# Kernel tuning notes

Hardware: AMD Instinct MI355X
Metric: run time of the kernel (lower is better)

The kernel has to match this reference:

```python
import jax, jax.numpy as jnp
import numpy as np

N_ATOMS = 50000
N_EDGES = 1_600_000
N_MOL = 500
HIDDEN = 128
FILTERS = 128
GAUSS = 50
LAYERS = 3
CUTOFF = 10.0
LOG2 = 0.6931471805599453


def ssp(x):
    # ShiftedSoftplus: softplus(x) - log(2)
    return jax.nn.softplus(x) - LOG2


def setup_inputs() -> dict:
    key = jax.random.key(0)
    ks = jax.random.split(key, 24)
    z = jax.random.randint(ks[0], (N_ATOMS,), 0, 100)
    pos = jax.random.uniform(ks[1], (N_ATOMS, 3), jnp.float32) * 5.0  # box keeps d < cutoff
    batch = jnp.sort(jax.random.randint(ks[2], (N_ATOMS,), 0, N_MOL))
    row = jax.random.randint(ks[3], (N_EDGES,), 0, N_ATOMS)
    off = jax.random.randint(ks[4], (N_EDGES,), 1, N_ATOMS)
    col = (row + off) % N_ATOMS  # guarantees row != col (no zero distances)
    edge_index = jnp.stack([row, col])
    def lin(k, fi, fo):
        return jax.random.normal(k, (fi, fo), jnp.float32) * (1.0 / np.sqrt(fi))
    emb = jax.random.normal(ks[5], (100, HIDDEN), jnp.float32)
    mlp1_w = jnp.stack([lin(jax.random.fold_in(ks[6], i), GAUSS, FILTERS) for i in range(LAYERS)])
    mlp1_b = jnp.zeros((LAYERS, FILTERS), jnp.float32)
    mlp2_w = jnp.stack([lin(jax.random.fold_in(ks[7], i), FILTERS, FILTERS) for i in range(LAYERS)])
    mlp2_b = jnp.zeros((LAYERS, FILTERS), jnp.float32)
    lin1_w = jnp.stack([lin(jax.random.fold_in(ks[8], i), HIDDEN, FILTERS) for i in range(LAYERS)])
    lin2_w = jnp.stack([lin(jax.random.fold_in(ks[9], i), FILTERS, HIDDEN) for i in range(LAYERS)])
    lin2_b = jnp.zeros((LAYERS, HIDDEN), jnp.float32)
    int_w = jnp.stack([lin(jax.random.fold_in(ks[10], i), HIDDEN, HIDDEN) for i in range(LAYERS)])
    int_b = jnp.zeros((LAYERS, HIDDEN), jnp.float32)
    out1_w = lin(ks[11], HIDDEN, HIDDEN // 2)
    out1_b = jnp.zeros((HIDDEN // 2,), jnp.float32)
    out2_w = lin(ks[12], HIDDEN // 2, 1)
    out2_b = jnp.zeros((1,), jnp.float32)
    return {"z": z, "pos": pos, "batch": batch, "edge_index": edge_index,
            "emb": emb, "mlp1_w": mlp1_w, "mlp1_b": mlp1_b, "mlp2_w": mlp2_w, "mlp2_b": mlp2_b,
            "lin1_w": lin1_w, "lin2_w": lin2_w, "lin2_b": lin2_b, "int_w": int_w, "int_b": int_b,
            "out1_w": out1_w, "out1_b": out1_b, "out2_w": out2_w, "out2_b": out2_b}


def reference(z, pos, batch, edge_index, emb, mlp1_w, mlp1_b, mlp2_w, mlp2_b,
              lin1_w, lin2_w, lin2_b, int_w, int_b, out1_w, out1_b, out2_w, out2_b):
    row, col = edge_index[0], edge_index[1]  # source j, target i
    d = jnp.linalg.norm(pos[row] - pos[col], axis=-1)  # [E]
    # GaussianSmearing
    offset = jnp.linspace(0.0, CUTOFF, GAUSS)
    coeff = -0.5 / (offset[1] - offset[0]) ** 2
    rbf = jnp.exp(coeff * (d[:, None] - offset[None, :]) ** 2)  # [E, GAUSS]
    # cosine cutoff
    C = 0.5 * (jnp.cos(d * jnp.pi / CUTOFF) + 1.0)  # [E]
    h = emb[z]  # [N, H]
    for l in range(LAYERS):
        W = ssp(rbf @ mlp1_w[l] + mlp1_b[l]) @ mlp2_w[l] + mlp2_b[l]  # [E, F]
        W = W * C[:, None]
        x = h @ lin1_w[l]                 # [N, F]
        msg = x[row] * W                  # gather from source, per-edge filter
        agg = jax.ops.segment_sum(msg, col, num_segments=N_ATOMS)  # scatter-add to targets
        x = agg @ lin2_w[l] + lin2_b[l]
        x = ssp(x)
        x = x @ int_w[l] + int_b[l]
        h = h + x                         # residual
    h = ssp(h @ out1_w + out1_b)
    h = h @ out2_w + out2_b               # [N, 1] per-atom energy
    out = jax.ops.segment_sum(h[:, 0], batch, num_segments=N_MOL)  # 'add' readout
    return out.reshape(-1)
```

## Files before the change

kernel.cpp:

```cpp
#include <hip/hip_runtime.h>
#include <math.h>

#define HID 128
#define NGAUSS 50
#define TBL 2048
#define TBL2 8192
#define DMAX 8.6605f
#define LDX 136
#define PGRID 768

typedef _Float16 h4 __attribute__((ext_vector_type(4)));
typedef _Float16 f16x8 __attribute__((ext_vector_type(8)));
typedef float f32x4 __attribute__((ext_vector_type(4)));

__device__ __forceinline__ float sspf(float x) {
  float ax = fabsf(x);
  return fmaxf(x, 0.0f) + log1pf(expf(-ax)) - 0.69314718055994530942f;
}

__global__ __launch_bounds__(128) void build_table_k(
    const float* __restrict__ w1, const float* __restrict__ b1,
    const float* __restrict__ w2, const float* __restrict__ b2,
    float* __restrict__ tab) {
  int l = blockIdx.x >> 11;
  int ti = blockIdx.x & (TBL - 1);
  int j = threadIdx.x;
  __shared__ float rbf[NGAUSS];
  __shared__ float v1[HID];
  const float step = DMAX / (float)(TBL - 1);
  float d = ti * step;
  if (j < NGAUSS) {
    const float gstep = 10.0f / 49.0f;
    const float gcoeff = -12.005f;
    float diff = d - j * gstep;
    rbf[j] = expf(gcoeff * diff * diff);
  }
  __syncthreads();
  float s = b1[l * HID + j];
  const float* w1p = w1 + l * NGAUSS * HID + j;
  for (int g = 0; g < NGAUSS; g++) s = fmaf(rbf[g], w1p[g * HID], s);
  v1[j] = sspf(s);
  __syncthreads();
  float s2 = b2[l * HID + j];
  const float* w2p = w2 + l * HID * HID + j;
  for (int k = 0; k < HID; k++) s2 = fmaf(v1[k], w2p[k * HID], s2);
  float C = 0.5f * (cosf(d * 0.3141592653589793f) + 1.0f);
  tab[((size_t)l * TBL + ti) * HID + j] = s2 * C;
}

__global__ __launch_bounds__(256) void upsample_k(
    const float* __restrict__ tab, _Float16* __restrict__ tabh) {
  int idx = blockIdx.x * 256 + threadIdx.x;
  if (idx >= 3 * TBL2 * HID) return;
  int ch = idx & 127;
  int i = (idx >> 7) & (TBL2 - 1);
  int l = idx >> 20;
  float t = (float)i * ((float)(TBL - 1) / (float)(TBL2 - 1));
  int i0 = min((int)t, TBL - 2);
  float f = t - (float)i0;
  const float* base = tab + ((size_t)l * TBL + i0) * HID + ch;
  tabh[idx] = (_Float16)fmaf(f, base[HID] - base[0], base[0]);
}

__global__ __launch_bounds__(256) void wswz10_k(
    const float* __restrict__ lin1, const float* __restrict__ lin2,
    const float* __restrict__ intw, const float* __restrict__ out1w,
    _Float16* __restrict__ out) {
  int b = blockIdx.x;
  int t = threadIdx.x;
  if (b < 9) {
    const float* src = (b < 3 ? lin1 : (b < 6 ? lin2 : intw)) + (size_t)(b % 3) * HID * HID;
    _Float16* dst = out + (size_t)b * 16384;
    for (int i = t; i < 16384; i += 256) {
      int j = i & 7;
      int lane = (i >> 3) & 63;
      int kk = (i >> 9) & 3;
      int ntc = i >> 11;
      int n = ntc * 16 + (lane & 15);
      int k = kk * 32 + (lane >> 4) * 8 + j;
      dst[i] = (_Float16)src[k * HID + n];
    }
  } else {
    _Float16* dst = out + (size_t)9 * 16384;
    for (int i = t; i < 8192; i += 256) {
      int j = i & 7;
      int lane = (i >> 3) & 63;
      int kk = (i >> 9) & 3;
      int ntc = i >> 11;
      int n = ntc * 16 + (lane & 15);
      int k = kk * 32 + (lane >> 4) * 8 + j;
      dst[i] = (_Float16)out1w[k * 64 + n];
    }
  }
}

__global__ __launch_bounds__(256) void emb_gather_k(
    const int* __restrict__ z, const float* __restrict__ emb,
    _Float16* __restrict__ h16, int N) {
  int i4 = blockIdx.x * 256 + threadIdx.x;
  if (i4 >= N * 32) return;
  int a = i4 >> 5;
  float4 v = ((const float4*)emb)[z[a] * 32 + (i4 & 31)];
  h4 o;
  o.x = (_Float16)v.x; o.y = (_Float16)v.y;
  o.z = (_Float16)v.z; o.w = (_Float16)v.w;
  ((h4*)h16)[i4] = o;
}

__global__ __launch_bounds__(256) void bcount_k(
    const int* __restrict__ col, int* __restrict__ bcount, int E, int nbuck) {
  __shared__ int hist[1024];
  int t = threadIdx.x;
  int e0 = blockIdx.x * 2048;
  for (int j = t; j < nbuck; j += 256) hist[j] = 0;
  __syncthreads();
#pragma unroll
  for (int u = 0; u < 8; u++) {
    int e = e0 + u * 256 + t;
    if (e < E) atomicAdd(&hist[col[e] >> 6], 1);
  }
  __syncthreads();
  for (int j = t; j < nbuck; j += 256)
    if (hist[j]) atomicAdd(&bcount[j], hist[j]);
}

__global__ __launch_bounds__(256) void bucket_scan_k(
    const int* __restrict__ bcount, int* __restrict__ bstart,
    int* __restrict__ bcur, int nbuck, int* __restrict__ starts, int N) {
  __shared__ int sh[256];
  int t = threadIdx.x;
  int chunk = (nbuck + 255) / 256;
  int b0 = t * chunk;
  int c[8];
  int s = 0;
  for (int j = 0; j < chunk; j++) {
    int idx = b0 + j;
    int v = (idx < nbuck) ? bcount[idx] : 0;
    c[j] = v;
    s += v;
  }
  sh[t] = s;
  __syncthreads();
  for (int o = 1; o < 256; o <<= 1) {
    int v = (t >= o) ? sh[t - o] : 0;
    __syncthreads();
    sh[t] += v;
    __syncthreads();
  }
  int p = (t == 0) ? 0 : sh[t - 1];
  for (int j = 0; j < chunk; j++) {
    int idx = b0 + j;
    if (idx < nbuck) {
      bstart[idx] = p;
      bcur[idx] = p;
      p += c[j];
    }
  }
  if (t == 255) {
    bstart[nbuck] = p;
    starts[N] = p;
  }
}

__global__ __launch_bounds__(256) void scatterA_k(
    const int* __restrict__ row, const int* __restrict__ col,
    const float* __restrict__ pos, int* __restrict__ bcur,
    unsigned long long* __restrict__ tmp, int E, int nbuck) {
  __shared__ int hist[1024];
  __shared__ int base[1024];
  int t = threadIdx.x;
  int e0 = blockIdx.x * 2048;
  for (int j = t; j < nbuck; j += 256) hist[j] = 0;
  __syncthreads();
  int bkt[8];
  int rnk[8];
  unsigned long long key[8];
#pragma unroll
  for (int u = 0; u < 8; u++) {
    int e = e0 + u * 256 + t;
    bkt[u] = -1;
    if (e < E) {
      int r = row[e], c = col[e];
      float dx = pos[r * 3 + 0] - pos[c * 3 + 0];
      float dy = pos[r * 3 + 1] - pos[c * 3 + 1];
      float dz = pos[r * 3 + 2] - pos[c * 3 + 2];
      float d = sqrtf(dx * dx + dy * dy + dz * dz);
      const float inv2 = (float)(TBL2 - 1) / DMAX;
      int q = min((int)(d * inv2 + 0.5f), TBL2 - 1);
      unsigned int pay = ((unsigned int)r << 13) | (unsigned int)q;
      key[u] = ((unsigned long long)pay << 6) | (unsigned long long)(c & 63);
      bkt[u] = c >> 6;
      rnk[u] = atomicAdd(&hist[bkt[u]], 1);
    }
  }
  __syncthreads();
  for (int j = t; j < nbuck; j += 256)
    base[j] = hist[j] ? atomicAdd(&bcur[j], hist[j]) : 0;
  __syncthreads();
#pragma unroll
  for (int u = 0; u < 8; u++)
    if (bkt[u] >= 0) tmp[(size_t)base[bkt[u]] + rnk[u]] = key[u];
}

__global__ __launch_bounds__(256) void scatterB_k(
    const unsigned long long* __restrict__ tmp, const int* __restrict__ bstart,
    int* __restrict__ starts, unsigned int* __restrict__ payload, int N) {
  int j = blockIdx.x;
  int t = threadIdx.x;
  __shared__ int cnt[64];
  __shared__ int cur[64];
  int rs = bstart[j], re = bstart[j + 1];
  if (t < 64) cnt[t] = 0;
  __syncthreads();
  for (int e = rs + t; e < re; e += 256)
    atomicAdd(&cnt[(int)(tmp[e] & 63)], 1);
  __syncthreads();
  if (t < 64) {
    int mine = cnt[t];
    int v = mine;
    for (int o = 1; o < 64; o <<= 1) {
      int u = __shfl_up(v, o, 64);
      if (t >= o) v += u;
    }
    int excl = v - mine;
    int c = j * 64 + t;
    if (c < N) starts[c] = rs + excl;
    cur[t] = rs + excl;
  }
  __syncthreads();
  for (int e = rs + t; e < re; e += 256) {
    unsigned long long k = tmp[e];
    int p = atomicAdd(&cur[(int)(k & 63)], 1);
    payload[p] = (unsigned int)(k >> 6);
  }
}


__global__ __launch_bounds__(256) void lin_p_k(
    const _Float16* __restrict__ in16, const _Float16* __restrict__ Wsw,
    _Float16* __restrict__ out16, int N, int ntiles) {
  __shared__ __align__(16) _Float16 Ws[16384];
  __shared__ __align__(16) _Float16 Xs[32 * LDX];
  __shared__ __align__(16) _Float16 Ys[32 * LDX];
  int t = threadIdx.x;
  int lane = t & 63, w = t >> 6;
  int g = w & 1, c = w >> 1;
  int mrow = lane & 15, quad = lane >> 4;
#pragma unroll
  for (int p = 0; p < 8; p++)
    ((uint4*)Ws)[t + p * 256] = ((const uint4*)Wsw)[t + p * 256];
  __syncthreads();
  f32x4 zero = {0.f, 0.f, 0.f, 0.f};
  for (int tile = blockIdx.x; tile < ntiles; tile += gridDim.x) {
    int a0 = tile * 32;
#pragma unroll
    for (int p = 0; p < 2; p++) {
      int id = t + p * 256;
      int a = id >> 4, kg = id & 15;
      uint4 v = make_uint4(0, 0, 0, 0);
      if (a0 + a < N) v = ((const uint4*)in16)[(size_t)(a0 + a) * 16 + kg];
      *(uint4*)&Xs[a * LDX + kg * 8] = v;
    }
    __syncthreads();
    f16x8 af[4];
#pragma unroll
    for (int kk = 0; kk < 4; kk++)
      af[kk] = *(const f16x8*)&Xs[(g * 16 + mrow) * LDX + kk * 32 + quad * 8];
    f32x4 acc[4];
#pragma unroll
    for (int i = 0; i < 4; i++) acc[i] = zero;
#pragma unroll
    for (int kk = 0; kk < 4; kk++) {
#pragma unroll
      for (int nt = 0; nt < 4; nt++) {
        f16x8 bf = *(const f16x8*)&Ws[(((c * 4 + nt) * 4 + kk) << 9) + lane * 8];
        acc[nt] = __builtin_amdgcn_mfma_f32_16x16x32_f16(af[kk], bf, acc[nt], 0, 0, 0);
      }
    }
#pragma unroll
    for (int nt = 0; nt < 4; nt++) {
      int colv = c * 64 + nt * 16 + mrow;
#pragma unroll
      for (int r = 0; r < 4; r++)
        Ys[(g * 16 + quad * 4 + r) * LDX + colv] = (_Float16)acc[nt][r];
    }
    __syncthreads();
#pragma unroll
    for (int p = 0; p < 2; p++) {
      int id = t + p * 256;
      int a = id >> 4, kg = id & 15;
      if (a0 + a < N)
        ((uint4*)out16)[(size_t)(a0 + a) * 16 + kg] = *(uint4*)&Ys[a * LDX + kg * 8];
    }
  }
}

__global__ __launch_bounds__(256) void ssp_p_k(
    const _Float16* __restrict__ agg16, const _Float16* __restrict__ Wsw,
    const float* __restrict__ bias, _Float16* __restrict__ y16, int N, int ntiles) {
  __shared__ __align__(16) _Float16 Ws[16384];
  __shared__ __align__(16) _Float16 Xs[32 * LDX];
  __shared__ __align__(16) _Float16 Ys[32 * LDX];
  int t = threadIdx.x;
  int lane = t & 63, w = t >> 6;
  int g = w & 1, c = w >> 1;
  int mrow = lane & 15, quad = lane >> 4;
#pragma unroll
  for (int p = 0; p < 8; p++)
    ((uint4*)Ws)[t + p * 256] = ((const uint4*)Wsw)[t + p * 256];
  float br[4];
#pragma unroll
  for (int nt = 0; nt < 4; nt++) br[nt] = bias[c * 64 + nt * 16 + mrow];
  __syncthreads();
  f32x4 zero = {0.f, 0.f, 0.f, 0.f};
  for (int tile = blockIdx.x; tile < ntiles; tile += gridDim.x) {
    int a0 = tile * 32;
#pragma unroll
    for (int p = 0; p < 2; p++) {
      int id = t + p * 256;
      int a = id >> 4, kg = id & 15;
      uint4 v = make_uint4(0, 0, 0, 0);
      if (a0 + a < N) v = ((const uint4*)agg16)[(size_t)(a0 + a) * 16 + kg];
      *(uint4*)&Xs[a * LDX + kg * 8] = v;
    }
    __syncthreads();
    f16x8 af[4];
#pragma unroll
    for (int kk = 0; kk < 4; kk++)
      af[kk] = *(const f16x8*)&Xs[(g * 16 + mrow) * LDX + kk * 32 + quad * 8];
    f32x4 acc[4];
#pragma unroll
    for (int i = 0; i < 4; i++) acc[i] = zero;
#pragma unroll
    for (int kk = 0; kk < 4; kk++) {
#pragma unroll
      for (int nt = 0; nt < 4; nt++) {
        f16x8 bf = *(const f16x8*)&Ws[(((c * 4 + nt) * 4 + kk) << 9) + lane * 8];
        acc[nt] = __builtin_amdgcn_mfma_f32_16x16x32_f16(af[kk], bf, acc[nt], 0, 0, 0);
      }
    }
#pragma unroll
    for (int nt = 0; nt < 4; nt++) {
      int colv = c * 64 + nt * 16 + mrow;
#pragma unroll
      for (int r = 0; r < 4; r++)
        Ys[(g * 16 + quad * 4 + r) * LDX + colv] = (_Float16)sspf(acc[nt][r] + br[nt]);
    }
    __syncthreads();
#pragma unroll
    for (int p = 0; p < 2; p++) {
      int id = t + p * 256;
      int a = id >> 4, kg = id & 15;
      if (a0 + a < N)
        ((uint4*)y16)[(size_t)(a0 + a) * 16 + kg] = *(uint4*)&Ys[a * LDX + kg * 8];
    }
  }
}

__global__ __launch_bounds__(256) void res_p_k(
    const _Float16* __restrict__ y16, const _Float16* __restrict__ Wsw,
    const float* __restrict__ bias, _Float16* __restrict__ h16, int N, int ntiles) {
  __shared__ __align__(16) _Float16 Ws[16384];
  __shared__ __align__(16) _Float16 Xs[32 * LDX];
  __shared__ __align__(16) _Float16 Ys[32 * LDX];
  int t = threadIdx.x;
  int lane = t & 63, w = t >> 6;
  int g = w & 1, c = w >> 1;
  int mrow = lane & 15, quad = lane >> 4;
#pragma unroll
  for (int p = 0; p < 8; p++)
    ((uint4*)Ws)[t + p * 256] = ((const uint4*)Wsw)[t + p * 256];
  float br[4];
#pragma unroll
  for (int nt = 0; nt < 4; nt++) br[nt] = bias[c * 64 + nt * 16 + mrow];
  __syncthreads();
  f32x4 zero = {0.f, 0.f, 0.f, 0.f};
  for (int tile = blockIdx.x; tile < ntiles; tile += gridDim.x) {
    int a0 = tile * 32;
#pragma unroll
    for (int p = 0; p < 2; p++) {
      int id = t + p * 256;
      int a = id >> 4, kg = id & 15;
      uint4 v = make_uint4(0, 0, 0, 0);
      if (a0 + a < N) v = ((const uint4*)y16)[(size_t)(a0 + a) * 16 + kg];
      *(uint4*)&Xs[a * LDX + kg * 8] = v;
    }
    __syncthreads();
    f16x8 af[4];
#pragma unroll
    for (int kk = 0; kk < 4; kk++)
      af[kk] = *(const f16x8*)&Xs[(g * 16 + mrow) * LDX + kk * 32 + quad * 8];
    f32x4 acc[4];
#pragma unroll
    for (int i = 0; i < 4; i++) acc[i] = zero;
#pragma unroll
    for (int kk = 0; kk < 4; kk++) {
#pragma unroll
      for (int nt = 0; nt < 4; nt++) {
        f16x8 bf = *(const f16x8*)&Ws[(((c * 4 + nt) * 4 + kk) << 9) + lane * 8];
        acc[nt] = __builtin_amdgcn_mfma_f32_16x16x32_f16(af[kk], bf, acc[nt], 0, 0, 0);
      }
    }
#pragma unroll
    for (int nt = 0; nt < 4; nt++) {
      int colv = c * 64 + nt * 16 + mrow;
#pragma unroll
      for (int r = 0; r < 4; r++)
        Ys[(g * 16 + quad * 4 + r) * LDX + colv] = (_Float16)(acc[nt][r] + br[nt]);
    }
    __syncthreads();
#pragma unroll
    for (int p = 0; p < 2; p++) {
      int id = t + p * 256;
      int a = id >> 4, kg = id & 15;
      if (a0 + a < N) {
        f16x8 hv = *(f16x8*)&((uint4*)h16)[(size_t)(a0 + a) * 16 + kg];
        f16x8 yv = *(f16x8*)&Ys[a * LDX + kg * 8];
        f16x8 o;
#pragma unroll
        for (int j = 0; j < 8; j++) o[j] = (_Float16)((float)hv[j] + (float)yv[j]);
        ((uint4*)h16)[(size_t)(a0 + a) * 16 + kg] = *(uint4*)&o;
      }
    }
  }
}

__global__ __launch_bounds__(256) void energy_p_k(
    const _Float16* __restrict__ h16, const _Float16* __restrict__ Wsw,
    const float* __restrict__ o1b, const float* __restrict__ o2w,
    const float* __restrict__ o2b, const int* __restrict__ batch,
    float* __restrict__ out, int N, int ntiles) {
  __shared__ __align__(16) _Float16 Ws[8192];
  __shared__ __align__(16) _Float16 Xs[32 * LDX];
  __shared__ float ebuf[32];
  __shared__ int bat[32];
  int t = threadIdx.x;
  int lane = t & 63, w = t >> 6;
  int g = w & 1, c = w >> 1;
  int mrow = lane & 15, quad = lane >> 4;
#pragma unroll
  for (int p = 0; p < 4; p++)
    ((uint4*)Ws)[t + p * 256] = ((const uint4*)Wsw)[t + p * 256];
  float br[2], wr[2];
#pragma unroll
  for (int nt = 0; nt < 2; nt++) {
    int colv = c * 32 + nt * 16 + mrow;
    br[nt] = o1b[colv];
    wr[nt] = o2w[colv];
  }
  float o2b0 = o2b[0];
  if (t < 32) ebuf[t] = 0.f;
  __syncthreads();
  f32x4 zero = {0.f, 0.f, 0.f, 0.f};
  for (int tile = blockIdx.x; tile < ntiles; tile += gridDim.x) {
    int a0 = tile * 32;
#pragma unroll
    for (int p = 0; p < 2; p++) {
      int id = t + p * 256;
      int a = id >> 4, kg = id & 15;
      uint4 v = make_uint4(0, 0, 0, 0);
      if (a0 + a < N) v = ((const uint4*)h16)[(size_t)(a0 + a) * 16 + kg];
      *(uint4*)&Xs[a * LDX + kg * 8] = v;
    }
    if (t < 32) bat[t] = (a0 + t < N) ? batch[a0 + t] : -1;
    __syncthreads();
    f16x8 af[4];
#pragma unroll
    for (int kk = 0; kk < 4; kk++)
      af[kk] = *(const f16x8*)&Xs[(g * 16 + mrow) * LDX + kk * 32 + quad * 8];
    f32x4 acc[2];
    acc[0] = zero; acc[1] = zero;
#pragma unroll
    for (int kk = 0; kk < 4; kk++) {
#pragma unroll
      for (int nt = 0; nt < 2; nt++) {
        f16x8 bf = *(const f16x8*)&Ws[(((c * 2 + nt) * 4 + kk) << 9) + lane * 8];
        acc[nt] = __builtin_amdgcn_mfma_f32_16x16x32_f16(af[kk], bf, acc[nt], 0, 0, 0);
      }
    }
    float ss[4] = {0.f, 0.f, 0.f, 0.f};
#pragma unroll
    for (int nt = 0; nt < 2; nt++)
#pragma unroll
      for (int r = 0; r < 4; r++) ss[r] += sspf(acc[nt][r] + br[nt]) * wr[nt];
#pragma unroll
    for (int r = 0; r < 4; r++) {
      ss[r] += __shfl_xor(ss[r], 1);
      ss[r] += __shfl_xor(ss[r], 2);
      ss[r] += __shfl_xor(ss[r], 4);
      ss[r] += __shfl_xor(ss[r], 8);
      if (mrow == 0) atomicAdd(&ebuf[g * 16 + quad * 4 + r], ss[r]);
    }
    __syncthreads();
    if (t == 0) {
      float acs = 0.f;
      int pm = -1;
      for (int i = 0; i < 32; i++) {
        int m = bat[i];
        float e = ebuf[i];
        ebuf[i] = 0.f;
        if (m < 0) break;
        if (m != pm) {
          if (pm >= 0) atomicAdd(&out[pm], acs);
          acs = 0.f;
          pm = m;
        }
        acs += e + o2b0;
      }
      if (pm >= 0) atomicAdd(&out[pm], acs);
    }
  }
}

__global__ __launch_bounds__(256) void aggregate_k(
    const int* __restrict__ starts, const unsigned int* __restrict__ payload,
    const _Float16* __restrict__ x16, const _Float16* __restrict__ tabh,
    _Float16* __restrict__ agg16, int N) {
  int a = blockIdx.x * 4 + (threadIdx.x >> 6);
  if (a >= N) return;
  int lane = threadIdx.x & 63;
  int half = lane >> 5;
  int sl = lane & 31;
  int s = starts[a], e_end = starts[a + 1];
  float4 acc0 = make_float4(0.f, 0.f, 0.f, 0.f);
  float4 acc1 = make_float4(0.f, 0.f, 0.f, 0.f);
  auto do_edge = [&](unsigned int p, float4& acc) {
    int tq = (int)(p & 8191u);
    int r = (int)(p >> 13);
    h4 tw = *(const h4*)&tabh[(size_t)tq * HID + sl * 4];
    h4 xr = *(const h4*)&x16[(size_t)r * HID + sl * 4];
    acc.x = fmaf((float)xr.x, (float)tw.x, acc.x);
    acc.y = fmaf((float)xr.y, (float)tw.y, acc.y);
    acc.z = fmaf((float)xr.z, (float)tw.z, acc.z);
    acc.w = fmaf((float)xr.w, (float)tw.w, acc.w);
  };
  int i = s;
  for (; i + 8 <= e_end; i += 8) {
    unsigned int p0 = payload[i + half];
    unsigned int p1 = payload[i + 2 + half];
    unsigned int p2 = payload[i + 4 + half];
    unsigned int p3 = payload[i + 6 + half];
    do_edge(p0, acc0);
    do_edge(p1, acc1);
    do_edge(p2, acc0);
    do_edge(p3, acc1);
  }
  for (; i < e_end; i += 2) {
    int e = i + half;
    if (e < e_end) do_edge(payload[e], acc0);
  }
  acc0.x += acc1.x; acc0.y += acc1.y; acc0.z += acc1.z; acc0.w += acc1.w;
  acc0.x += __shfl_xor(acc0.x, 32);
  acc0.y += __shfl_xor(acc0.y, 32);
  acc0.z += __shfl_xor(acc0.z, 32);
  acc0.w += __shfl_xor(acc0.w, 32);
  if (half == 0) {
    h4 o;
    o.x = (_Float16)acc0.x; o.y = (_Float16)acc0.y;
    o.z = (_Float16)acc0.z; o.w = (_Float16)acc0.w;
    *(h4*)&agg16[(size_t)a * HID + sl * 4] = o;
  }
}

extern "C" void kernel_launch(void* const* d_in, const int* in_sizes, int n_in,
                              void* d_out, int out_size, void* d_ws, size_t ws_size,
                              hipStream_t stream) {
  const int* z = (const int*)d_in[0];
  const float* pos = (const float*)d_in[1];
  const int* batch = (const int*)d_in[2];
  const int* eidx = (const int*)d_in[3];
  const float* emb = (const float*)d_in[4];
  const float* mlp1_w = (const float*)d_in[5];
  const float* mlp1_b = (const float*)d_in[6];
  const float* mlp2_w = (const float*)d_in[7];
  const float* mlp2_b = (const float*)d_in[8];
  const float* lin1_w = (const float*)d_in[9];
  const float* lin2_w = (const float*)d_in[10];
  const float* lin2_b = (const float*)d_in[11];
  const float* int_w = (const float*)d_in[12];
  const float* int_b = (const float*)d_in[13];
  const float* out1_w = (const float*)d_in[14];
  const float* out1_b = (const float*)d_in[15];
  const float* out2_w = (const float*)d_in[16];
  const float* out2_b = (const float*)d_in[17];
  float* out = (float*)d_out;

  const int N = in_sizes[0];
  const int E = in_sizes[3] / 2;
  const int* row = eidx;
  const int* col = eidx + E;
  const int nbuck = (N + 63) / 64;
  const int ntiles = (N + 31) / 32;

  char* ws = (char*)d_ws;
  size_t off = 0;
  auto alloc = [&](size_t bytes) -> void* {
    void* p = ws + off;
    off = (off + bytes + 255) & ~(size_t)255;
    return p;
  };
  _Float16* h16 = (_Float16*)alloc((size_t)N * HID * 2);
  _Float16* x16 = (_Float16*)alloc((size_t)N * HID * 2);
  size_t agg_bytes = (size_t)N * HID * 2;
  size_t tmp_bytes = (size_t)E * 8 + 16;
  void* agg_union = alloc(agg_bytes > tmp_bytes ? agg_bytes : tmp_bytes);
  _Float16* agg16 = (_Float16*)agg_union;
  unsigned long long* tmp = (unsigned long long*)agg_union;
  unsigned int* payload = (unsigned int*)alloc((size_t)E * 4 + 16);
  int* starts = (int*)alloc((size_t)(N + 1) * 4);
  int* bcount = (int*)alloc((size_t)nbuck * 4);
  int* bstart = (int*)alloc((size_t)(nbuck + 1) * 4);
  int* bcur = (int*)alloc((size_t)nbuck * 4);
  float* tab = (float*)alloc((size_t)3 * TBL * HID * 4);
  _Float16* tabh = (_Float16*)alloc((size_t)3 * TBL2 * HID * 2);
  _Float16* Wsw = (_Float16*)alloc((size_t)10 * 16384 * 2);
  (void)ws_size;

  hipMemsetAsync(bcount, 0, (size_t)nbuck * 4, stream);
  hipMemsetAsync(out, 0, (size_t)out_size * 4, stream);

  build_table_k<<<3 * TBL, 128, 0, stream>>>(mlp1_w, mlp1_b, mlp2_w, mlp2_b, tab);
  upsample_k<<<(3 * TBL2 * HID + 255) / 256, 256, 0, stream>>>(tab, tabh);
  wswz10_k<<<10, 256, 0, stream>>>(lin1_w, lin2_w, int_w, out1_w, Wsw);
  emb_gather_k<<<(N * 32 + 255) / 256, 256, 0, stream>>>(z, emb, h16, N);
  bcount_k<<<(E + 2047) / 2048, 256, 0, stream>>>(col, bcount, E, nbuck);
  bucket_scan_k<<<1, 256, 0, stream>>>(bcount, bstart, bcur, nbuck, starts, N);
  scatterA_k<<<(E + 2047) / 2048, 256, 0, stream>>>(row, col, pos, bcur, tmp, E, nbuck);
  scatterB_k<<<nbuck, 256, 0, stream>>>(tmp, bstart, starts, payload, N);

  int pg = PGRID < ntiles ? PGRID : ntiles;
  for (int l = 0; l < 3; l++) {
    lin_p_k<<<pg, 256, 0, stream>>>(h16, Wsw + (size_t)l * 16384, x16, N, ntiles);
    aggregate_k<<<(N + 3) / 4, 256, 0, stream>>>(starts, payload, x16,
                                                 tabh + (size_t)l * TBL2 * HID, agg16, N);
    ssp_p_k<<<pg, 256, 0, stream>>>(agg16, Wsw + (size_t)(3 + l) * 16384,
                                    lin2_b + (size_t)l * HID, x16, N, ntiles);
    res_p_k<<<pg, 256, 0, stream>>>(x16, Wsw + (size_t)(6 + l) * 16384,
                                    int_b + (size_t)l * HID, h16, N, ntiles);
  }
  energy_p_k<<<pg, 256, 0, stream>>>(h16, Wsw + (size_t)9 * 16384, out1_b, out2_w,
                                     out2_b, batch, out, N, ntiles);
}
```

Baseline: 561.8 us.

## Fuse per-layer node MLPs and next-layer lin1 into one kernel

Replaces the separate ssp, residual and lin1 node-GEMM kernels with a single layer kernel. Each wave handles 16 rows across all 128 columns, reading weights straight from global/L2 instead of staging them in LDS. The intermediate activations stay in a per-wave LDS slice, and the next layer's lin1 product is computed in the same pass. This cuts launches, intermediate HBM round trips and block-level barriers, at the cost of more VGPRs (8 accumulators) and uncached global weight fetches per MFMA.

```diff
diff --git a/kernel.cpp b/kernel.cpp
--- a/kernel.cpp
+++ b/kernel.cpp
@@ -237,189 +237,144 @@
 
 
 __global__ __launch_bounds__(256) void lin_p_k(
-    const _Float16* __restrict__ in16, const _Float16* __restrict__ Wsw,
+    const _Float16* __restrict__ in16, const _Float16* __restrict__ Wg,
     _Float16* __restrict__ out16, int N, int ntiles) {
-  __shared__ __align__(16) _Float16 Ws[16384];
-  __shared__ __align__(16) _Float16 Xs[32 * LDX];
-  __shared__ __align__(16) _Float16 Ys[32 * LDX];
+  __shared__ __align__(16) _Float16 Sl[64 * LDX];
   int t = threadIdx.x;
   int lane = t & 63, w = t >> 6;
-  int g = w & 1, c = w >> 1;
   int mrow = lane & 15, quad = lane >> 4;
-#pragma unroll
-  for (int p = 0; p < 8; p++)
-    ((uint4*)Ws)[t + p * 256] = ((const uint4*)Wsw)[t + p * 256];
-  __syncthreads();
+  _Float16* sl = Sl + w * 16 * LDX;
   f32x4 zero = {0.f, 0.f, 0.f, 0.f};
   for (int tile = blockIdx.x; tile < ntiles; tile += gridDim.x) {
-    int a0 = tile * 32;
-#pragma unroll
-    for (int p = 0; p < 2; p++) {
-      int id = t + p * 256;
-      int a = id >> 4, kg = id & 15;
-      uint4 v = make_uint4(0, 0, 0, 0);
-      if (a0 + a < N) v = ((const uint4*)in16)[(size_t)(a0 + a) * 16 + kg];
-      *(uint4*)&Xs[a * LDX + kg * 8] = v;
-    }
-    __syncthreads();
+    int r0 = tile * 64 + w * 16;
+    int ar = min(r0 + mrow, N - 1);
     f16x8 af[4];
 #pragma unroll
     for (int kk = 0; kk < 4; kk++)
-      af[kk] = *(const f16x8*)&Xs[(g * 16 + mrow) * LDX + kk * 32 + quad * 8];
-    f32x4 acc[4];
-#pragma unroll
-    for (int i = 0; i < 4; i++) acc[i] = zero;
-#pragma unroll
-    for (int kk = 0; kk < 4; kk++) {
-#pragma unroll
-      for (int nt = 0; nt < 4; nt++) {
-        f16x8 bf = *(const f16x8*)&Ws[(((c * 4 + nt) * 4 + kk) << 9) + lane * 8];
+      af[kk] = *(const f16x8*)(in16 + (size_t)ar * HID + kk * 32 + quad * 8);
+    f32x4 acc[8];
+#pragma unroll
+    for (int i = 0; i < 8; i++) acc[i] = zero;
+#pragma unroll
+    for (int kk = 0; kk < 4; kk++)
+#pragma unroll
+      for (int nt = 0; nt < 8; nt++) {
+        f16x8 bf = *(const f16x8*)(Wg + (((nt * 4 + kk) << 9) + lane * 8));
         acc[nt] = __builtin_amdgcn_mfma_f32_16x16x32_f16(af[kk], bf, acc[nt], 0, 0, 0);
       }
-    }
-#pragma unroll
-    for (int nt = 0; nt < 4; nt++) {
-      int colv = c * 64 + nt * 16 + mrow;
+#pragma unroll
+    for (int nt = 0; nt < 8; nt++)
 #pragma unroll
       for (int r = 0; r < 4; r++)
-        Ys[(g * 16 + quad * 4 + r) * LDX + colv] = (_Float16)acc[nt][r];
-    }
-    __syncthreads();
-#pragma unroll
-    for (int p = 0; p < 2; p++) {
-      int id = t + p * 256;
-      int a = id >> 4, kg = id & 15;
-      if (a0 + a < N)
-        ((uint4*)out16)[(size_t)(a0 + a) * 16 + kg] = *(uint4*)&Ys[a * LDX + kg * 8];
-    }
-  }
-}
-
-__global__ __launch_bounds__(256) void ssp_p_k(
-    const _Float16* __restrict__ agg16, const _Float16* __restrict__ Wsw,
-    const float* __restrict__ bias, _Float16* __restrict__ y16, int N, int ntiles) {
-  __shared__ __align__(16) _Float16 Ws[16384];
-  __shared__ __align__(16) _Float16 Xs[32 * LDX];
-  __shared__ __align__(16) _Float16 Ys[32 * LDX];
+        sl[(quad * 4 + r) * LDX + nt * 16 + mrow] = (_Float16)acc[nt][r];
+#pragma unroll
+    for (int p = 0; p < 4; p++) {
+      int idx = lane + p * 64;
+      int rr = idx >> 4, kg = idx & 15;
+      int a = r0 + rr;
+      if (a < N)
+        ((uint4*)out16)[(size_t)a * 16 + kg] = *(uint4*)&sl[rr * LDX + kg * 8];
+    }
+  }
+}
+
+__global__ __launch_bounds__(256) void layer_p_k(
+    const _Float16* __restrict__ agg16, const _Float16* __restrict__ W2g,
+    const float* __restrict__ b2, const _Float16* __restrict__ W3g,
+    const float* __restrict__ b3, _Float16* __restrict__ h16,
+    const _Float16* __restrict__ W1g, _Float16* __restrict__ x16,
+    int N, int ntiles, int do_lin) {
+  __shared__ __align__(16) _Float16 Sl[64 * LDX];
   int t = threadIdx.x;
   int lane = t & 63, w = t >> 6;
-  int g = w & 1, c = w >> 1;
   int mrow = lane & 15, quad = lane >> 4;
-#pragma unroll
-  for (int p = 0; p < 8; p++)
-    ((uint4*)Ws)[t + p * 256] = ((const uint4*)Wsw)[t + p * 256];
-  float br[4];
-#pragma unroll
-  for (int nt = 0; nt < 4; nt++) br[nt] = bias[c * 64 + nt * 16 + mrow];
-  __syncthreads();
+  _Float16* sl = Sl + w * 16 * LDX;
+  float br2[8], br3[8];
+#pragma unroll
+  for (int nt = 0; nt < 8; nt++) {
+    br2[nt] = b2[nt * 16 + mrow];
+    br3[nt] = b3[nt * 16 + mrow];
+  }
   f32x4 zero = {0.f, 0.f, 0.f, 0.f};
   for (int tile = blockIdx.x; tile < ntiles; tile += gridDim.x) {
-    int a0 = tile * 32;
-#pragma unroll
-    for (int p = 0; p < 2; p++) {
-      int id = t + p * 256;
-      int a = id >> 4, kg = id & 15;
-      uint4 v = make_uint4(0, 0, 0, 0);
-      if (a0 + a < N) v = ((const uint4*)agg16)[(size_t)(a0 + a) * 16 + kg];
-      *(uint4*)&Xs[a * LDX + kg * 8] = v;
-    }
-    __syncthreads();
+    int r0 = tile * 64 + w * 16;
+    int ar = min(r0 + mrow, N - 1);
     f16x8 af[4];
 #pragma unroll
     for (int kk = 0; kk < 4; kk++)
-      af[kk] = *(const f16x8*)&Xs[(g * 16 + mrow) * LDX + kk * 32 + quad * 8];
-    f32x4 acc[4];
-#pragma unroll
-    for (int i = 0; i < 4; i++) acc[i] = zero;
-#pragma unroll
-    for (int kk = 0; kk < 4; kk++) {
-#pragma unroll
-      for (int nt = 0; nt < 4; nt++) {
-        f16x8 bf = *(const f16x8*)&Ws[(((c * 4 + nt) * 4 + kk) << 9) + lane * 8];
+      af[kk] = *(const f16x8*)(agg16 + (size_t)ar * HID + kk * 32 + quad * 8);
+    f32x4 acc[8];
+#pragma unroll
+    for (int i = 0; i < 8; i++) acc[i] = zero;
+#pragma unroll
+    for (int kk = 0; kk < 4; kk++)
+#pragma unroll
+      for (int nt = 0; nt < 8; nt++) {
+        f16x8 bf = *(const f16x8*)(W2g + (((nt * 4 + kk) << 9) + lane * 8));
         acc[nt] = __builtin_amdgcn_mfma_f32_16x16x32_f16(af[kk], bf, acc[nt], 0, 0, 0);
       }
-    }
-#pragma unroll
-    for (int nt = 0; nt < 4; nt++) {
-      int colv = c * 64 + nt * 16 + mrow;
+#pragma unroll
+    for (int nt = 0; nt < 8; nt++)
 #pragma unroll
       for (int r = 0; r < 4; r++)
-        Ys[(g * 16 + quad * 4 + r) * LDX + colv] = (_Float16)sspf(acc[nt][r] + br[nt]);
-    }
-    __syncthreads();
-#pragma unroll
-    for (int p = 0; p < 2; p++) {
-      int id = t + p * 256;
-      int a = id >> 4, kg = id & 15;
-      if (a0 + a < N)
-        ((uint4*)y16)[(size_t)(a0 + a) * 16 + kg] = *(uint4*)&Ys[a * LDX + kg * 8];
-    }
-  }
-}
-
-__global__ __launch_bounds__(256) void res_p_k(
-    const _Float16* __restrict__ y16, const _Float16* __restrict__ Wsw,
-    const float* __restrict__ bias, _Float16* __restrict__ h16, int N, int ntiles) {
-  __shared__ __align__(16) _Float16 Ws[16384];
-  __shared__ __align__(16) _Float16 Xs[32 * LDX];
-  __shared__ __align__(16) _Float16 Ys[32 * LDX];
-  int t = threadIdx.x;
-  int lane = t & 63, w = t >> 6;
-  int g = w & 1, c = w >> 1;
-  int mrow = lane & 15, quad = lane >> 4;
-#pragma unroll
-  for (int p = 0; p < 8; p++)
-    ((uint4*)Ws)[t + p * 256] = ((const uint4*)Wsw)[t + p * 256];
-  float br[4];
-#pragma unroll
-  for (int nt = 0; nt < 4; nt++) br[nt] = bias[c * 64 + nt * 16 + mrow];
-  __syncthreads();
-  f32x4 zero = {0.f, 0.f, 0.f, 0.f};
-  for (int tile = blockIdx.x; tile < ntiles; tile += gridDim.x) {
-    int a0 = tile * 32;
-#pragma unroll
-    for (int p = 0; p < 2; p++) {
-      int id = t + p * 256;
-      int a = id >> 4, kg = id & 15;
-      uint4 v = make_uint4(0, 0, 0, 0);
-      if (a0 + a < N) v = ((const uint4*)y16)[(size_t)(a0 + a) * 16 + kg];
-      *(uint4*)&Xs[a * LDX + kg * 8] = v;
-    }
-    __syncthreads();
-    f16x8 af[4];
+        sl[(quad * 4 + r) * LDX + nt * 16 + mrow] = (_Float16)sspf(acc[nt][r] + br2[nt]);
 #pragma unroll
     for (int kk = 0; kk < 4; kk++)
-      af[kk] = *(const f16x8*)&Xs[(g * 16 + mrow) * LDX + kk * 32 + quad * 8];
-    f32x4 acc[4];
-#pragma unroll
-    for (int i = 0; i < 4; i++) acc[i] = zero;
-#pragma unroll
-    for (int kk = 0; kk < 4; kk++) {
-#pragma unroll
-      for (int nt = 0; nt < 4; nt++) {
-        f16x8 bf = *(const f16x8*)&Ws[(((c * 4 + nt) * 4 + kk) << 9) + lane * 8];
+      af[kk] = *(const f16x8*)&sl[mrow * LDX + kk * 32 + quad * 8];
+#pragma unroll
+    for (int i = 0; i < 8; i++) acc[i] = zero;
+#pragma unroll
+    for (int kk = 0; kk < 4; kk++)
+#pragma unroll
+      for (int nt = 0; nt < 8; nt++) {
+        f16x8 bf = *(const f16x8*)(W3g + (((nt * 4 + kk) << 9) + lane * 8));
         acc[nt] = __builtin_amdgcn_mfma_f32_16x16x32_f16(af[kk], bf, acc[nt], 0, 0, 0);
       }
-    }
-#pragma unroll
-    for (int nt = 0; nt < 4; nt++) {
-      int colv = c * 64 + nt * 16 + mrow;
+#pragma unroll
+    for (int nt = 0; nt < 8; nt++)
 #pragma unroll
       for (int r = 0; r < 4; r++)
-        Ys[(g * 16 + quad * 4 + r) * LDX + colv] = (_Float16)(acc[nt][r] + br[nt]);
-    }
-    __syncthreads();
-#pragma unroll
-    for (int p = 0; p < 2; p++) {
-      int id = t + p * 256;
-      int a = id >> 4, kg = id & 15;
-      if (a0 + a < N) {
-        f16x8 hv = *(f16x8*)&((uint4*)h16)[(size_t)(a0 + a) * 16 + kg];
-        f16x8 yv = *(f16x8*)&Ys[a * LDX + kg * 8];
+        sl[(quad * 4 + r) * LDX + nt * 16 + mrow] = (_Float16)(acc[nt][r] + br3[nt]);
+#pragma unroll
+    for (int p = 0; p < 4; p++) {
+      int idx = lane + p * 64;
+      int rr = idx >> 4, kg = idx & 15;
+      int a = r0 + rr;
+      if (a < N) {
+        f16x8 yv = *(f16x8*)&sl[rr * LDX + kg * 8];
+        f16x8 hv = *(const f16x8*)&((const uint4*)h16)[(size_t)a * 16 + kg];
         f16x8 o;
 #pragma unroll
         for (int j = 0; j < 8; j++) o[j] = (_Float16)((float)hv[j] + (float)yv[j]);
-        ((uint4*)h16)[(size_t)(a0 + a) * 16 + kg] = *(uint4*)&o;
+        ((uint4*)h16)[(size_t)a * 16 + kg] = *(uint4*)&o;
+        *(f16x8*)&sl[rr * LDX + kg * 8] = o;
+      }
+    }
+    if (do_lin) {
+#pragma unroll
+      for (int kk = 0; kk < 4; kk++)
+        af[kk] = *(const f16x8*)&sl[mrow * LDX + kk * 32 + quad * 8];
+#pragma unroll
+      for (int i = 0; i < 8; i++) acc[i] = zero;
+#pragma unroll
+      for (int kk = 0; kk < 4; kk++)
+#pragma unroll
+        for (int nt = 0; nt < 8; nt++) {
+          f16x8 bf = *(const f16x8*)(W1g + (((nt * 4 + kk) << 9) + lane * 8));
+          acc[nt] = __builtin_amdgcn_mfma_f32_16x16x32_f16(af[kk], bf, acc[nt], 0, 0, 0);
+        }
+#pragma unroll
+      for (int nt = 0; nt < 8; nt++)
+#pragma unroll
+        for (int r = 0; r < 4; r++)
+          sl[(quad * 4 + r) * LDX + nt * 16 + mrow] = (_Float16)acc[nt][r];
+#pragma unroll
+      for (int p = 0; p < 4; p++) {
+        int idx = lane + p * 64;
+        int rr = idx >> 4, kg = idx & 15;
+        int a = r0 + rr;
+        if (a < N)
+          ((uint4*)x16)[(size_t)a * 16 + kg] = *(uint4*)&sl[rr * LDX + kg * 8];
       }
     }
   }
@@ -590,7 +545,8 @@
   const int* row = eidx;
   const int* col = eidx + E;
   const int nbuck = (N + 63) / 64;
-  const int ntiles = (N + 31) / 32;
+  const int nt64 = (N + 63) / 64;
+  const int nt32 = (N + 31) / 32;
 
   char* ws = (char*)d_ws;
   size_t off = 0;
@@ -628,16 +584,17 @@
   scatterA_k<<<(E + 2047) / 2048, 256, 0, stream>>>(row, col, pos, bcur, tmp, E, nbuck);
   scatterB_k<<<nbuck, 256, 0, stream>>>(tmp, bstart, starts, payload, N);
 
-  int pg = PGRID < ntiles ? PGRID : ntiles;
+  int pg = PGRID < nt64 ? PGRID : nt64;
+  lin_p_k<<<pg, 256, 0, stream>>>(h16, Wsw, x16, N, nt64);
   for (int l = 0; l < 3; l++) {
-    lin_p_k<<<pg, 256, 0, stream>>>(h16, Wsw + (size_t)l * 16384, x16, N, ntiles);
     aggregate_k<<<(N + 3) / 4, 256, 0, stream>>>(starts, payload, x16,
                                                  tabh + (size_t)l * TBL2 * HID, agg16, N);
-    ssp_p_k<<<pg, 256, 0, stream>>>(agg16, Wsw + (size_t)(3 + l) * 16384,
-                                    lin2_b + (size_t)l * HID, x16, N, ntiles);
-    res_p_k<<<pg, 256, 0, stream>>>(x16, Wsw + (size_t)(6 + l) * 16384,
-                                    int_b + (size_t)l * HID, h16, N, ntiles);
-  }
-  energy_p_k<<<pg, 256, 0, stream>>>(h16, Wsw + (size_t)9 * 16384, out1_b, out2_w,
-                                     out2_b, batch, out, N, ntiles);
-}
+    layer_p_k<<<pg, 256, 0, stream>>>(
+        agg16, Wsw + (size_t)(3 + l) * 16384, lin2_b + (size_t)l * HID,
+        Wsw + (size_t)(6 + l) * 16384, int_b + (size_t)l * HID, h16,
+        Wsw + (size_t)(l + 1) * 16384, x16, N, nt64, (l < 2) ? 1 : 0);
+  }
+  int pg32 = PGRID < nt32 ? PGRID : nt32;
+  energy_p_k<<<pg32, 256, 0, stream>>>(h16, Wsw + (size_t)9 * 16384, out1_b, out2_w,
+                                       out2_b, batch, out, N, nt32);
+}
```

Result: slower. 634.4 us (+12.9%).

## Read GEMM weights from global memory and accumulate aggregation in packed fp16

Applied to the files above, without the earlier changes.

The node-level GEMM kernels stop staging the weight matrix in LDS and read MFMA B-fragments straight from global memory (L2/L1 cached), with launch bounds asking for 4 blocks per CU. This cuts LDS use per block and removes the per-block weight copy and barrier. Separately, the edge aggregation kernel now accumulates products in packed fp16 over groups of 8 edges per half-wave before flushing to fp32, which reduces conversion and FMA instruction count at some cost in precision. The change risks lower accuracy and extra global traffic for weights.

```diff
diff --git a/kernel.cpp b/kernel.cpp
--- a/kernel.cpp
+++ b/kernel.cpp
@@ -236,20 +236,15 @@
 }
 
 
-__global__ __launch_bounds__(256) void lin_p_k(
-    const _Float16* __restrict__ in16, const _Float16* __restrict__ Wsw,
+__global__ __launch_bounds__(256, 4) void lin_p_k(
+    const _Float16* __restrict__ in16, const _Float16* __restrict__ Wg,
     _Float16* __restrict__ out16, int N, int ntiles) {
-  __shared__ __align__(16) _Float16 Ws[16384];
   __shared__ __align__(16) _Float16 Xs[32 * LDX];
   __shared__ __align__(16) _Float16 Ys[32 * LDX];
   int t = threadIdx.x;
   int lane = t & 63, w = t >> 6;
   int g = w & 1, c = w >> 1;
   int mrow = lane & 15, quad = lane >> 4;
-#pragma unroll
-  for (int p = 0; p < 8; p++)
-    ((uint4*)Ws)[t + p * 256] = ((const uint4*)Wsw)[t + p * 256];
-  __syncthreads();
   f32x4 zero = {0.f, 0.f, 0.f, 0.f};
   for (int tile = blockIdx.x; tile < ntiles; tile += gridDim.x) {
     int a0 = tile * 32;
@@ -273,7 +268,7 @@
     for (int kk = 0; kk < 4; kk++) {
 #pragma unroll
       for (int nt = 0; nt < 4; nt++) {
-        f16x8 bf = *(const f16x8*)&Ws[(((c * 4 + nt) * 4 + kk) << 9) + lane * 8];
+        f16x8 bf = *(const f16x8*)(Wg + ((((c * 4 + nt) * 4 + kk) << 9) + lane * 8));
         acc[nt] = __builtin_amdgcn_mfma_f32_16x16x32_f16(af[kk], bf, acc[nt], 0, 0, 0);
       }
     }
@@ -295,23 +290,18 @@
   }
 }
 
-__global__ __launch_bounds__(256) void ssp_p_k(
-    const _Float16* __restrict__ agg16, const _Float16* __restrict__ Wsw,
+__global__ __launch_bounds__(256, 4) void ssp_p_k(
+    const _Float16* __restrict__ agg16, const _Float16* __restrict__ Wg,
     const float* __restrict__ bias, _Float16* __restrict__ y16, int N, int ntiles) {
-  __shared__ __align__(16) _Float16 Ws[16384];
   __shared__ __align__(16) _Float16 Xs[32 * LDX];
   __shared__ __align__(16) _Float16 Ys[32 * LDX];
   int t = threadIdx.x;
   int lane = t & 63, w = t >> 6;
   int g = w & 1, c = w >> 1;
   int mrow = lane & 15, quad = lane >> 4;
-#pragma unroll
-  for (int p = 0; p < 8; p++)
-    ((uint4*)Ws)[t + p * 256] = ((const uint4*)Wsw)[t + p * 256];
   float br[4];
 #pragma unroll
   for (int nt = 0; nt < 4; nt++) br[nt] = bias[c * 64 + nt * 16 + mrow];
-  __syncthreads();
   f32x4 zero = {0.f, 0.f, 0.f, 0.f};
   for (int tile = blockIdx.x; tile < ntiles; tile += gridDim.x) {
     int a0 = tile * 32;
@@ -335,7 +325,7 @@
     for (int kk = 0; kk < 4; kk++) {
 #pragma unroll
       for (int nt = 0; nt < 4; nt++) {
-        f16x8 bf = *(const f16x8*)&Ws[(((c * 4 + nt) * 4 + kk) << 9) + lane * 8];
+        f16x8 bf = *(const f16x8*)(Wg + ((((c * 4 + nt) * 4 + kk) << 9) + lane * 8));
         acc[nt] = __builtin_amdgcn_mfma_f32_16x16x32_f16(af[kk], bf, acc[nt], 0, 0, 0);
       }
     }
@@ -357,23 +347,18 @@
   }
 }
 
-__global__ __launch_bounds__(256) void res_p_k(
-    const _Float16* __restrict__ y16, const _Float16* __restrict__ Wsw,
+__global__ __launch_bounds__(256, 4) void res_p_k(
+    const _Float16* __restrict__ y16, const _Float16* __restrict__ Wg,
     const float* __restrict__ bias, _Float16* __restrict__ h16, int N, int ntiles) {
-  __shared__ __align__(16) _Float16 Ws[16384];
   __shared__ __align__(16) _Float16 Xs[32 * LDX];
   __shared__ __align__(16) _Float16 Ys[32 * LDX];
   int t = threadIdx.x;
   int lane = t & 63, w = t >> 6;
   int g = w & 1, c = w >> 1;
   int mrow = lane & 15, quad = lane >> 4;
-#pragma unroll
-  for (int p = 0; p < 8; p++)
-    ((uint4*)Ws)[t + p * 256] = ((const uint4*)Wsw)[t + p * 256];
   float br[4];
 #pragma unroll
   for (int nt = 0; nt < 4; nt++) br[nt] = bias[c * 64 + nt * 16 + mrow];
-  __syncthreads();
   f32x4 zero = {0.f, 0.f, 0.f, 0.f};
   for (int tile = blockIdx.x; tile < ntiles; tile += gridDim.x) {
     int a0 = tile * 32;
@@ -397,7 +382,7 @@
     for (int kk = 0; kk < 4; kk++) {
 #pragma unroll
       for (int nt = 0; nt < 4; nt++) {
-        f16x8 bf = *(const f16x8*)&Ws[(((c * 4 + nt) * 4 + kk) << 9) + lane * 8];
+        f16x8 bf = *(const f16x8*)(Wg + ((((c * 4 + nt) * 4 + kk) << 9) + lane * 8));
         acc[nt] = __builtin_amdgcn_mfma_f32_16x16x32_f16(af[kk], bf, acc[nt], 0, 0, 0);
       }
     }
@@ -414,7 +399,7 @@
       int id = t + p * 256;
       int a = id >> 4, kg = id & 15;
       if (a0 + a < N) {
-        f16x8 hv = *(f16x8*)&((uint4*)h16)[(size_t)(a0 + a) * 16 + kg];
+        f16x8 hv = *(const f16x8*)&((const uint4*)h16)[(size_t)(a0 + a) * 16 + kg];
         f16x8 yv = *(f16x8*)&Ys[a * LDX + kg * 8];
         f16x8 o;
 #pragma unroll
@@ -425,12 +410,11 @@
   }
 }
 
-__global__ __launch_bounds__(256) void energy_p_k(
-    const _Float16* __restrict__ h16, const _Float16* __restrict__ Wsw,
+__global__ __launch_bounds__(256, 4) void energy_p_k(
+    const _Float16* __restrict__ h16, const _Float16* __restrict__ Wg,
     const float* __restrict__ o1b, const float* __restrict__ o2w,
     const float* __restrict__ o2b, const int* __restrict__ batch,
     float* __restrict__ out, int N, int ntiles) {
-  __shared__ __align__(16) _Float16 Ws[8192];
   __shared__ __align__(16) _Float16 Xs[32 * LDX];
   __shared__ float ebuf[32];
   __shared__ int bat[32];
@@ -438,9 +422,6 @@
   int lane = t & 63, w = t >> 6;
   int g = w & 1, c = w >> 1;
   int mrow = lane & 15, quad = lane >> 4;
-#pragma unroll
-  for (int p = 0; p < 4; p++)
-    ((uint4*)Ws)[t + p * 256] = ((const uint4*)Wsw)[t + p * 256];
   float br[2], wr[2];
 #pragma unroll
   for (int nt = 0; nt < 2; nt++) {
@@ -474,7 +455,7 @@
     for (int kk = 0; kk < 4; kk++) {
 #pragma unroll
       for (int nt = 0; nt < 2; nt++) {
-        f16x8 bf = *(const f16x8*)&Ws[(((c * 2 + nt) * 4 + kk) << 9) + lane * 8];
+        f16x8 bf = *(const f16x8*)(Wg + ((((c * 2 + nt) * 4 + kk) << 9) + lane * 8));
         acc[nt] = __builtin_amdgcn_mfma_f32_16x16x32_f16(af[kk], bf, acc[nt], 0, 0, 0);
       }
     }
@@ -522,42 +503,49 @@
   int half = lane >> 5;
   int sl = lane & 31;
   int s = starts[a], e_end = starts[a + 1];
-  float4 acc0 = make_float4(0.f, 0.f, 0.f, 0.f);
-  float4 acc1 = make_float4(0.f, 0.f, 0.f, 0.f);
-  auto do_edge = [&](unsigned int p, float4& acc) {
+  float4 accf = make_float4(0.f, 0.f, 0.f, 0.f);
+  const h4 z4 = {(_Float16)0.f, (_Float16)0.f, (_Float16)0.f, (_Float16)0.f};
+  auto do_edge = [&](unsigned int p, h4& acc) {
     int tq = (int)(p & 8191u);
     int r = (int)(p >> 13);
     h4 tw = *(const h4*)&tabh[(size_t)tq * HID + sl * 4];
     h4 xr = *(const h4*)&x16[(size_t)r * HID + sl * 4];
-    acc.x = fmaf((float)xr.x, (float)tw.x, acc.x);
-    acc.y = fmaf((float)xr.y, (float)tw.y, acc.y);
-    acc.z = fmaf((float)xr.z, (float)tw.z, acc.z);
-    acc.w = fmaf((float)xr.w, (float)tw.w, acc.w);
+    acc += tw * xr;
+  };
+  auto flush = [&](h4 a0, h4 a1) {
+    accf.x += (float)a0.x + (float)a1.x;
+    accf.y += (float)a0.y + (float)a1.y;
+    accf.z += (float)a0.z + (float)a1.z;
+    accf.w += (float)a0.w + (float)a1.w;
   };
   int i = s;
-  for (; i + 8 <= e_end; i += 8) {
-    unsigned int p0 = payload[i + half];
-    unsigned int p1 = payload[i + 2 + half];
-    unsigned int p2 = payload[i + 4 + half];
-    unsigned int p3 = payload[i + 6 + half];
-    do_edge(p0, acc0);
-    do_edge(p1, acc1);
-    do_edge(p2, acc0);
-    do_edge(p3, acc1);
-  }
-  for (; i < e_end; i += 2) {
-    int e = i + half;
-    if (e < e_end) do_edge(payload[e], acc0);
-  }
-  acc0.x += acc1.x; acc0.y += acc1.y; acc0.z += acc1.z; acc0.w += acc1.w;
-  acc0.x += __shfl_xor(acc0.x, 32);
-  acc0.y += __shfl_xor(acc0.y, 32);
-  acc0.z += __shfl_xor(acc0.z, 32);
-  acc0.w += __shfl_xor(acc0.w, 32);
+  for (; i + 16 <= e_end; i += 16) {
+    h4 a0 = z4, a1 = z4;
+    do_edge(payload[i + half], a0);
+    do_edge(payload[i + 2 + half], a1);
+    do_edge(payload[i + 4 + half], a0);
+    do_edge(payload[i + 6 + half], a1);
+    do_edge(payload[i + 8 + half], a0);
+    do_edge(payload[i + 10 + half], a1);
+    do_edge(payload[i + 12 + half], a0);
+    do_edge(payload[i + 14 + half], a1);
+    flush(a0, a1);
+  }
+  {
+    h4 a0 = z4, a1 = z4;
+    int k = 0;
+    for (; i + 2 <= e_end; i += 2, k++) do_edge(payload[i + half], (k & 1) ? a1 : a0);
+    if (i < e_end && half == 0) do_edge(payload[i], a0);
+    flush(a0, a1);
+  }
+  accf.x += __shfl_xor(accf.x, 32);
+  accf.y += __shfl_xor(accf.y, 32);
+  accf.z += __shfl_xor(accf.z, 32);
+  accf.w += __shfl_xor(accf.w, 32);
   if (half == 0) {
     h4 o;
-    o.x = (_Float16)acc0.x; o.y = (_Float16)acc0.y;
-    o.z = (_Float16)acc0.z; o.w = (_Float16)acc0.w;
+    o.x = (_Float16)accf.x; o.y = (_Float16)accf.y;
+    o.z = (_Float16)accf.z; o.w = (_Float16)accf.w;
     *(h4*)&agg16[(size_t)a * HID + sl * 4] = o;
   }
 }
```

Result: no change. 555.3 us (-1.2%).
